# Kernel tuning notes

Hardware: AMD Instinct MI355X
Metric: run time of the kernel (lower is better)

Reference implementation:

```python
import jax, jax.numpy as jnp
import numpy as np

# ---- Build Cayley tables for projective GA G(3,0,1), basis ordered by grade ----
_BLADES = [(), (0,), (1,), (2,), (3,), (0,1), (0,2), (0,3), (1,2), (1,3), (2,3),
           (0,1,2), (0,1,3), (0,2,3), (1,2,3), (0,1,2,3)]
_IDX = {b: i for i, b in enumerate(_BLADES)}

def _blade_mul(a, b, metric):
    """Multiply basis blades a*b. Returns (sign, result_blade); sign=0 if it vanishes."""
    arr = list(a) + list(b)
    sign = 1
    changed = True
    while changed:
        changed = False
        for i in range(len(arr) - 1):
            if arr[i] > arr[i + 1]:
                arr[i], arr[i + 1] = arr[i + 1], arr[i]
                sign = -sign
                changed = True
            elif arr[i] == arr[i + 1]:
                sign *= metric[arr[i]]
                del arr[i:i + 2]
                changed = True
                break
    return sign, tuple(arr)

def _build_tables():
    metric = [0, 1, 1, 1]  # e0^2 = 0 (degenerate), e1^2=e2^2=e3^2=1
    G = np.zeros((16, 16, 16), np.float32)  # geometric product
    W = np.zeros((16, 16, 16), np.float32)  # outer (wedge) product
    for a in _BLADES:
        for b in _BLADES:
            s, r = _blade_mul(a, b, metric)
            if s != 0:
                G[_IDX[a], _IDX[b], _IDX[r]] = s
            if not (set(a) & set(b)):
                s2, r2 = _blade_mul(a, b, [1, 1, 1, 1])
                W[_IDX[a], _IDX[b], _IDX[r2]] = s2
    # Right-complement dual: dual(e_a) = s * e_c with e_a ^ dual(e_a) = e0123
    full = (0, 1, 2, 3)
    dual_idx = np.zeros(16, np.int32)
    dual_sign = np.zeros(16, np.float32)
    for a in _BLADES:
        c = tuple(sorted(set(full) - set(a)))
        s, _ = _blade_mul(a, c, [1, 1, 1, 1])
        dual_idx[_IDX[a]] = _IDX[c]
        dual_sign[_IDX[a]] = s
    # Coefficient map: dual(x)[j] = dual_sign[dual_idx[j]] * x[dual_idx[j]]
    out_sign = dual_sign[dual_idx]
    return jnp.asarray(G), jnp.asarray(W), jnp.asarray(dual_idx), jnp.asarray(out_sign)

_G, _W, _DUAL_IDX, _DUAL_SIGN = _build_tables()
_PSS = 15  # index of pseudoscalar e0123

def _dual(x):
    return x[..., _DUAL_IDX] * _DUAL_SIGN


def setup_inputs() -> dict:
    key = jax.random.key(0)
    k1, k2, k3 = jax.random.split(key, 3)
    B, T, C = 64, 8192, 16
    return {
        "x": jax.random.normal(k1, (B, T, C), dtype=jnp.float32),
        "y": jax.random.normal(k2, (B, T, C), dtype=jnp.float32),
        "ref": jax.random.normal(k3, (B, T, C), dtype=jnp.float32),
    }


def reference(x, y, ref):
    # Geometric product over the Cayley table
    gp = jnp.einsum("bti,btj,ijk->btk", x, y, _G)
    # E(3)-equivariant join: ref_e0123 * dual(dual(x) ^ dual(y))
    wedge = jnp.einsum("bti,btj,ijk->btk", _dual(x), _dual(y), _W)
    join = ref[..., _PSS:_PSS + 1] * _dual(wedge)
    return jnp.concatenate([gp, join], axis=-1)  # (B, T, 32)
```

## Files before the change

kernel.cpp:

```cpp
#include <hip/hip_runtime.h>

namespace ga {

constexpr int MASK[16]        = {0,1,2,4,8,3,5,9,6,10,12,7,11,13,14,15};
constexpr int IDX_OF_MASK[16] = {0,1,2,5,3,6,8,11,4,7,9,12,10,13,14,15};

constexpr int popc(int v) { int c = 0; while (v) { c += v & 1; v >>= 1; } return c; }

constexpr int reorder_sign(int a, int b) {
    int s = 0; int t = a >> 1;
    while (t) { s += popc(t & b); t >>= 1; }
    return (s & 1) ? -1 : 1;
}

struct Term { signed char i, j, k, s; };

struct GPTab { Term t[192]; };
constexpr GPTab build_gp() {
    GPTab T{}; int n = 0;
    for (int i = 0; i < 16; i++)
        for (int j = 0; j < 16; j++) {
            int a = MASK[i], b = MASK[j];
            if (a & b & 1) continue;
            T.t[n].i = (signed char)i;
            T.t[n].j = (signed char)j;
            T.t[n].k = (signed char)IDX_OF_MASK[a ^ b];
            T.t[n].s = (signed char)reorder_sign(a, b);
            n++;
        }
    return T;
}

struct JNTab { Term t[81]; };
constexpr JNTab build_join() {
    JNTab T{}; int n = 0;
    int didx[16] = {}, dsgn[16] = {};
    for (int i = 0; i < 16; i++) {
        int a = MASK[i], c = (~a) & 0xF;
        didx[i] = IDX_OF_MASK[c];
        dsgn[i] = reorder_sign(a, c);
    }
    for (int i = 0; i < 16; i++)
        for (int j = 0; j < 16; j++) {
            int p = didx[i], q = didx[j];
            int a = MASK[p], b = MASK[q];
            if (a & b) continue;
            int m = IDX_OF_MASK[a | b];
            int k = didx[m];
            int s = dsgn[i] * dsgn[j] * dsgn[m] * reorder_sign(a, b);
            T.t[n].i = (signed char)i;
            T.t[n].j = (signed char)j;
            T.t[n].k = (signed char)k;
            T.t[n].s = (signed char)s;
            n++;
        }
    return T;
}

constexpr GPTab G = build_gp();
constexpr JNTab J = build_join();

}

__global__ __launch_bounds__(256)
void MVGeometricBilinear_kernel(const float* __restrict__ x,
                                const float* __restrict__ y,
                                const float* __restrict__ ref,
                                float* __restrict__ out,
                                int npts)
{
    int pt = blockIdx.x * 256 + threadIdx.x;
    if (pt >= npts) return;

    const float4* xp = reinterpret_cast<const float4*>(x) + (size_t)pt * 4;
    const float4* yp = reinterpret_cast<const float4*>(y) + (size_t)pt * 4;

    float4 a0 = xp[0], a1 = xp[1], a2 = xp[2], a3 = xp[3];
    float4 b0 = yp[0], b1 = yp[1], b2 = yp[2], b3 = yp[3];
    float r = ref[(size_t)pt * 16 + 15];

    float xx[16] = {a0.x, a0.y, a0.z, a0.w, a1.x, a1.y, a1.z, a1.w,
                    a2.x, a2.y, a2.z, a2.w, a3.x, a3.y, a3.z, a3.w};
    float yy[16] = {b0.x, b0.y, b0.z, b0.w, b1.x, b1.y, b1.z, b1.w,
                    b2.x, b2.y, b2.z, b2.w, b3.x, b3.y, b3.z, b3.w};

    float gp[16] = {0.f, 0.f, 0.f, 0.f, 0.f, 0.f, 0.f, 0.f,
                    0.f, 0.f, 0.f, 0.f, 0.f, 0.f, 0.f, 0.f};
    float jn[16] = {0.f, 0.f, 0.f, 0.f, 0.f, 0.f, 0.f, 0.f,
                    0.f, 0.f, 0.f, 0.f, 0.f, 0.f, 0.f, 0.f};

#pragma unroll
    for (int t = 0; t < 192; t++) {
        const int ti = ga::G.t[t].i, tj = ga::G.t[t].j, tk = ga::G.t[t].k;
        const float v = xx[ti] * yy[tj];
        if (ga::G.t[t].s > 0) gp[tk] += v; else gp[tk] -= v;
    }
#pragma unroll
    for (int t = 0; t < 81; t++) {
        const int ti = ga::J.t[t].i, tj = ga::J.t[t].j, tk = ga::J.t[t].k;
        const float v = xx[ti] * yy[tj];
        if (ga::J.t[t].s > 0) jn[tk] += v; else jn[tk] -= v;
    }

    float4* op = reinterpret_cast<float4*>(out) + (size_t)pt * 8;
    op[0] = make_float4(gp[0],  gp[1],  gp[2],  gp[3]);
    op[1] = make_float4(gp[4],  gp[5],  gp[6],  gp[7]);
    op[2] = make_float4(gp[8],  gp[9],  gp[10], gp[11]);
    op[3] = make_float4(gp[12], gp[13], gp[14], gp[15]);
    op[4] = make_float4(r * jn[0],  r * jn[1],  r * jn[2],  r * jn[3]);
    op[5] = make_float4(r * jn[4],  r * jn[5],  r * jn[6],  r * jn[7]);
    op[6] = make_float4(r * jn[8],  r * jn[9],  r * jn[10], r * jn[11]);
    op[7] = make_float4(r * jn[12], r * jn[13], r * jn[14], r * jn[15]);
}

extern "C" void kernel_launch(void* const* d_in, const int* in_sizes, int n_in,
                              void* d_out, int out_size, void* d_ws, size_t ws_size,
                              hipStream_t stream) {
    const float* x   = (const float*)d_in[0];
    const float* y   = (const float*)d_in[1];
    const float* ref = (const float*)d_in[2];
    float* out = (float*)d_out;

    const int npts = in_sizes[0] / 16;
    const int blocks = (npts + 255) / 256;

    MVGeometricBilinear_kernel<<<blocks, 256, 0, stream>>>(x, y, ref, out, npts);
}
```

Measured before the change: 158.4 us.

## Stage loads and stores through LDS for fully coalesced global access

Each wave loads 64 points of x, y and ref as contiguous float4s into padded LDS, then each lane reads back its own point; outputs are staged the same way before a coalesced write. Blocks shrink to 128 threads, and a separate tail kernel covers points that do not fill a whole wave. The aim is to replace the per-thread strided 64-byte and 128-byte accesses with contiguous wave-wide transactions. The cost is extra LDS traffic, a block barrier, and reading the full ref rows instead of a single float.

Result: faster. 149.3 us (-5.7%).

```diff
diff --git a/kernel.cpp b/kernel.cpp
--- a/kernel.cpp
+++ b/kernel.cpp
@@ -62,55 +62,129 @@
 
 }
 
-__global__ __launch_bounds__(256)
+constexpr int XSTRIDE = 20;
+constexpr int OSTRIDE = 36;
+constexpr int WAVE_FLOATS = 64 * XSTRIDE * 2 + 64;
+
+__global__ __launch_bounds__(128)
 void MVGeometricBilinear_kernel(const float* __restrict__ x,
                                 const float* __restrict__ y,
                                 const float* __restrict__ ref,
                                 float* __restrict__ out,
-                                int npts)
+                                int nwaves)
 {
-    int pt = blockIdx.x * 256 + threadIdx.x;
-    if (pt >= npts) return;
-
-    const float4* xp = reinterpret_cast<const float4*>(x) + (size_t)pt * 4;
-    const float4* yp = reinterpret_cast<const float4*>(y) + (size_t)pt * 4;
-
-    float4 a0 = xp[0], a1 = xp[1], a2 = xp[2], a3 = xp[3];
-    float4 b0 = yp[0], b1 = yp[1], b2 = yp[2], b3 = yp[3];
-    float r = ref[(size_t)pt * 16 + 15];
-
-    float xx[16] = {a0.x, a0.y, a0.z, a0.w, a1.x, a1.y, a1.z, a1.w,
-                    a2.x, a2.y, a2.z, a2.w, a3.x, a3.y, a3.z, a3.w};
-    float yy[16] = {b0.x, b0.y, b0.z, b0.w, b1.x, b1.y, b1.z, b1.w,
-                    b2.x, b2.y, b2.z, b2.w, b3.x, b3.y, b3.z, b3.w};
-
+    __shared__ __align__(16) float lds[2 * WAVE_FLOATS];
+
+    const int wave = threadIdx.x >> 6;
+    const int lane = threadIdx.x & 63;
+    const long wid = (long)blockIdx.x * 2 + wave;
+    const bool active = (wid < nwaves);
+
+    float* wl = lds + wave * WAVE_FLOATS;
+    float* lx = wl;
+    float* ly = wl + 64 * XSTRIDE;
+    float* lr = wl + 128 * XSTRIDE;
+    float* lo = wl;
+
+    const long wbase = (active ? wid : 0) * 64;
+
+    float xx[16], yy[16], r = 0.f;
     float gp[16] = {0.f, 0.f, 0.f, 0.f, 0.f, 0.f, 0.f, 0.f,
                     0.f, 0.f, 0.f, 0.f, 0.f, 0.f, 0.f, 0.f};
     float jn[16] = {0.f, 0.f, 0.f, 0.f, 0.f, 0.f, 0.f, 0.f,
                     0.f, 0.f, 0.f, 0.f, 0.f, 0.f, 0.f, 0.f};
 
+    if (active) {
+        const float4* gx = reinterpret_cast<const float4*>(x)   + wbase * 4;
+        const float4* gy = reinterpret_cast<const float4*>(y)   + wbase * 4;
+        const float4* gr = reinterpret_cast<const float4*>(ref) + wbase * 4;
+#pragma unroll
+        for (int c = 0; c < 4; c++) {
+            const int g  = lane + 64 * c;
+            const int p  = g >> 2;
+            const int ch = g & 3;
+            const float4 vx = gx[g];
+            const float4 vy = gy[g];
+            const float4 vr = gr[g];
+            *reinterpret_cast<float4*>(lx + p * XSTRIDE + ch * 4) = vx;
+            *reinterpret_cast<float4*>(ly + p * XSTRIDE + ch * 4) = vy;
+            if (ch == 3) lr[p] = vr.w;
+        }
+
+#pragma unroll
+        for (int k = 0; k < 4; k++) {
+            const float4 vx = *reinterpret_cast<const float4*>(lx + lane * XSTRIDE + k * 4);
+            const float4 vy = *reinterpret_cast<const float4*>(ly + lane * XSTRIDE + k * 4);
+            xx[4*k+0] = vx.x; xx[4*k+1] = vx.y; xx[4*k+2] = vx.z; xx[4*k+3] = vx.w;
+            yy[4*k+0] = vy.x; yy[4*k+1] = vy.y; yy[4*k+2] = vy.z; yy[4*k+3] = vy.w;
+        }
+        r = lr[lane];
+
+#pragma unroll
+        for (int t = 0; t < 192; t++) {
+            const int ti = ga::G.t[t].i, tj = ga::G.t[t].j, tk = ga::G.t[t].k;
+            const float v = xx[ti] * yy[tj];
+            if (ga::G.t[t].s > 0) gp[tk] += v; else gp[tk] -= v;
+        }
+#pragma unroll
+        for (int t = 0; t < 81; t++) {
+            const int ti = ga::J.t[t].i, tj = ga::J.t[t].j, tk = ga::J.t[t].k;
+            const float v = xx[ti] * yy[tj];
+            if (ga::J.t[t].s > 0) jn[tk] += v; else jn[tk] -= v;
+        }
+    }
+
+    __syncthreads();
+
+    if (active) {
+#pragma unroll
+        for (int k = 0; k < 4; k++)
+            *reinterpret_cast<float4*>(lo + lane * OSTRIDE + k * 4) =
+                make_float4(gp[4*k+0], gp[4*k+1], gp[4*k+2], gp[4*k+3]);
+#pragma unroll
+        for (int k = 0; k < 4; k++)
+            *reinterpret_cast<float4*>(lo + lane * OSTRIDE + 16 + k * 4) =
+                make_float4(r * jn[4*k+0], r * jn[4*k+1], r * jn[4*k+2], r * jn[4*k+3]);
+
+        float4* go = reinterpret_cast<float4*>(out) + wbase * 8;
+#pragma unroll
+        for (int c = 0; c < 8; c++) {
+            const int g  = lane + 64 * c;
+            const int p  = g >> 3;
+            const int ch = g & 7;
+            go[g] = *reinterpret_cast<const float4*>(lo + p * OSTRIDE + ch * 4);
+        }
+    }
+}
+
+__global__ __launch_bounds__(64)
+void MVGeometricBilinear_tail(const float* __restrict__ x,
+                              const float* __restrict__ y,
+                              const float* __restrict__ ref,
+                              float* __restrict__ out,
+                              int start, int npts)
+{
+    int pt = start + blockIdx.x * 64 + threadIdx.x;
+    if (pt >= npts) return;
+    float xx[16], yy[16];
+#pragma unroll
+    for (int k = 0; k < 16; k++) { xx[k] = x[(size_t)pt*16+k]; yy[k] = y[(size_t)pt*16+k]; }
+    const float r = ref[(size_t)pt*16+15];
+    float gp[16] = {}, jn[16] = {};
 #pragma unroll
     for (int t = 0; t < 192; t++) {
-        const int ti = ga::G.t[t].i, tj = ga::G.t[t].j, tk = ga::G.t[t].k;
-        const float v = xx[ti] * yy[tj];
-        if (ga::G.t[t].s > 0) gp[tk] += v; else gp[tk] -= v;
+        const float v = xx[ga::G.t[t].i] * yy[ga::G.t[t].j];
+        if (ga::G.t[t].s > 0) gp[ga::G.t[t].k] += v; else gp[ga::G.t[t].k] -= v;
     }
 #pragma unroll
     for (int t = 0; t < 81; t++) {
-        const int ti = ga::J.t[t].i, tj = ga::J.t[t].j, tk = ga::J.t[t].k;
-        const float v = xx[ti] * yy[tj];
-        if (ga::J.t[t].s > 0) jn[tk] += v; else jn[tk] -= v;
-    }
-
-    float4* op = reinterpret_cast<float4*>(out) + (size_t)pt * 8;
-    op[0] = make_float4(gp[0],  gp[1],  gp[2],  gp[3]);
-    op[1] = make_float4(gp[4],  gp[5],  gp[6],  gp[7]);
-    op[2] = make_float4(gp[8],  gp[9],  gp[10], gp[11]);
-    op[3] = make_float4(gp[12], gp[13], gp[14], gp[15]);
-    op[4] = make_float4(r * jn[0],  r * jn[1],  r * jn[2],  r * jn[3]);
-    op[5] = make_float4(r * jn[4],  r * jn[5],  r * jn[6],  r * jn[7]);
-    op[6] = make_float4(r * jn[8],  r * jn[9],  r * jn[10], r * jn[11]);
-    op[7] = make_float4(r * jn[12], r * jn[13], r * jn[14], r * jn[15]);
+        const float v = xx[ga::J.t[t].i] * yy[ga::J.t[t].j];
+        if (ga::J.t[t].s > 0) jn[ga::J.t[t].k] += v; else jn[ga::J.t[t].k] -= v;
+    }
+#pragma unroll
+    for (int k = 0; k < 16; k++) out[(size_t)pt*32+k] = gp[k];
+#pragma unroll
+    for (int k = 0; k < 16; k++) out[(size_t)pt*32+16+k] = r * jn[k];
 }
 
 extern "C" void kernel_launch(void* const* d_in, const int* in_sizes, int n_in,
@@ -121,8 +195,15 @@
     const float* ref = (const float*)d_in[2];
     float* out = (float*)d_out;
 
-    const int npts = in_sizes[0] / 16;
-    const int blocks = (npts + 255) / 256;
-
-    MVGeometricBilinear_kernel<<<blocks, 256, 0, stream>>>(x, y, ref, out, npts);
-}
+    const int npts   = in_sizes[0] / 16;
+    const int nwaves = npts / 64;
+    const int blocks = (nwaves + 1) / 2;
+
+    MVGeometricBilinear_kernel<<<blocks, 128, 0, stream>>>(x, y, ref, out, nwaves);
+
+    const int rem = npts - nwaves * 64;
+    if (rem > 0) {
+        MVGeometricBilinear_tail<<<(rem + 63) / 64, 64, 0, stream>>>(
+            x, y, ref, out, nwaves * 64, npts);
+    }
+}
```
